# Kernel optimization log

Measured on AMD Instinct MI355X. Metric: run time of the kernel, lower is better.

Reference implementation:

```python
import jax, jax.numpy as jnp
import numpy as np
import math

B, T, D = 4, 8192, 1024
EPS = 1e-5

def setup_inputs() -> dict:
    key = jax.random.key(0)
    ks = jax.random.split(key, 8)
    xavier = lambda k, shape: jax.random.uniform(k, shape, jnp.float32,
                                                 -math.sqrt(6.0 / (shape[0] + shape[1])),
                                                 math.sqrt(6.0 / (shape[0] + shape[1])))
    x = jax.random.normal(ks[0], (B, T, D), jnp.float32)
    ln_gamma = jnp.ones((D,), jnp.float32)
    ln_beta = jnp.zeros((D,), jnp.float32)
    Wg = xavier(ks[1], (D, D))            # torch Linear weight: (out, in)
    bg = jnp.zeros((D,), jnp.float32)
    Wv = 0.01 * xavier(ks[2], (D, D))     # gain=0.01
    bv = jnp.zeros((D,), jnp.float32)
    Wo = 0.01 * xavier(ks[3], (D, D))     # gain=0.01
    bo = jnp.zeros((D,), jnp.float32)
    log_decay = jnp.asarray(math.log(math.exp(0.01) - 1.0), jnp.float32)
    return {"x": x, "ln_gamma": ln_gamma, "ln_beta": ln_beta,
            "Wg": Wg, "bg": bg, "Wv": Wv, "bv": bv, "Wo": Wo, "bo": bo,
            "log_decay": log_decay}

def reference(x, ln_gamma, ln_beta, Wg, bg, Wv, bv, Wo, bo, log_decay):
    # LayerNorm
    mu = jnp.mean(x, axis=-1, keepdims=True)
    var = jnp.mean(jnp.square(x - mu), axis=-1, keepdims=True)
    normed = (x - mu) * jax.lax.rsqrt(var + EPS) * ln_gamma + ln_beta
    # gate / value projections (torch Linear: y = x @ W.T + b)
    g = jax.nn.sigmoid(jnp.einsum('btd,ed->bte', normed, Wg) + bg)
    v = jnp.einsum('btd,ed->bte', normed, Wv) + bv
    # push-pull cumulative sums over time
    cumsum = jnp.cumsum(g * v, axis=1) - jnp.cumsum((1.0 - g) * v, axis=1)
    # positional exponential decay
    alpha = jax.nn.softplus(log_decay)
    positions = jnp.arange(x.shape[1], dtype=jnp.float32)
    decay = jnp.exp(-alpha * positions)[None, :, None]  # (1,T,1)
    out = jnp.einsum('btd,ed->bte', cumsum * decay, Wo) + bo
    return x + out  # dropout is identity at eval
```

## Files before the change

### kernel.cpp

```cpp
#include <hip/hip_runtime.h>
#include <cstdint>
#include <cstddef>

#define DD 1024
#define TT 8192
#define BB 4
#define MM (BB*TT)
#define NCHUNK 64
#define CLEN 128
#define EPS 1e-5f
#define NK2 16

typedef __attribute__((ext_vector_type(8))) short bf16x8;
typedef __attribute__((ext_vector_type(4))) float f32x4;

__device__ __forceinline__ float bf2f(unsigned short b) {
  union { unsigned int u; float f; } c; c.u = ((unsigned int)b) << 16; return c.f;
}
__device__ __forceinline__ unsigned short f2bf(float f) {
  union { float f; unsigned int u; } c; c.f = f;
  unsigned int lsb = (c.u >> 16) & 1u;
  c.u += 0x7fffu + lsb;
  return (unsigned short)(c.u >> 16);
}

__device__ __forceinline__ void gload16(const void* gsrc, void* ldst) {
  __builtin_amdgcn_global_load_lds(
      (const __attribute__((address_space(1))) unsigned int*)gsrc,
      (__attribute__((address_space(3))) unsigned int*)ldst, 16, 0, 0);
}

#define SWZ(row) (((row) >> 1) & 3)

__device__ __forceinline__ bf16x8 ldsfrag(const unsigned short* lds, int row, int sl) {
  int sp = sl ^ SWZ(row);
  return *(const bf16x8*)&lds[row * 32 + sp * 8];
}

#define MFMA16(a, b, c) __builtin_amdgcn_mfma_f32_16x16x32_bf16((a), (b), (c), 0, 0, 0)

#define VMCNT4 asm volatile("s_waitcnt vmcnt(4)" ::: "memory")
#define VMCNT0 asm volatile("s_waitcnt vmcnt(0)" ::: "memory")
#define BAR    __builtin_amdgcn_s_barrier()

__global__ __launch_bounds__(256) void cast_weights(
    const float* __restrict__ wg, const float* __restrict__ wv,
    const float* __restrict__ wo,
    unsigned short* __restrict__ owg, unsigned short* __restrict__ owv,
    unsigned short* __restrict__ owo) {
  int i = blockIdx.x * 256 + threadIdx.x;
  const float* src; unsigned short* dst; int off;
  if (i < 262144)       { src = wg; dst = owg; off = i; }
  else if (i < 524288)  { src = wv; dst = owv; off = i - 262144; }
  else                  { src = wo; dst = owo; off = i - 524288; }
  float4 v = ((const float4*)src)[off];
  ushort4 o;
  o.x = f2bf(v.x); o.y = f2bf(v.y); o.z = f2bf(v.z); o.w = f2bf(v.w);
  ((ushort4*)dst)[off] = o;
}

__global__ __launch_bounds__(256) void ln_kernel(
    const float* __restrict__ x, const float* __restrict__ gamma,
    const float* __restrict__ beta, unsigned short* __restrict__ normed) {
  size_t row = blockIdx.x;
  int tid = threadIdx.x, lane = tid & 63, wid = tid >> 6;
  float4 v = ((const float4*)(x + row * DD))[tid];
  float s = v.x + v.y + v.z + v.w;
  float q = v.x * v.x + v.y * v.y + v.z * v.z + v.w * v.w;
#pragma unroll
  for (int off = 32; off; off >>= 1) {
    s += __shfl_down(s, off);
    q += __shfl_down(q, off);
  }
  __shared__ float rs[4], rq[4];
  if (lane == 0) { rs[wid] = s; rq[wid] = q; }
  __syncthreads();
  float ts = rs[0] + rs[1] + rs[2] + rs[3];
  float tq = rq[0] + rq[1] + rq[2] + rq[3];
  float mu  = ts * (1.0f / DD);
  float var = tq * (1.0f / DD) - mu * mu;
  float rstd = rsqrtf(var + EPS);
  float4 gm = ((const float4*)gamma)[tid];
  float4 bt = ((const float4*)beta)[tid];
  ushort4 o;
  o.x = f2bf((v.x - mu) * rstd * gm.x + bt.x);
  o.y = f2bf((v.y - mu) * rstd * gm.y + bt.y);
  o.z = f2bf((v.z - mu) * rstd * gm.z + bt.z);
  o.w = f2bf((v.w - mu) * rstd * gm.w + bt.w);
  ((ushort4*)normed)[row * (DD / 4) + tid] = o;
}

__global__ __launch_bounds__(512, 2) void gemm_gv(
    const unsigned short* __restrict__ normed,
    const unsigned short* __restrict__ wg, const unsigned short* __restrict__ wv,
    const float* __restrict__ bg, const float* __restrict__ bv,
    unsigned short* __restrict__ u, float* __restrict__ sums) {
  __shared__ unsigned short As[2][2][256 * 32];
  __shared__ unsigned short Bgs[2][2][128 * 32];
  __shared__ unsigned short Bvs[2][2][128 * 32];
  int tid = threadIdx.x, lane = tid & 63, wid = tid >> 6;
  int wm = wid >> 2, wn = wid & 3;
  int nwg = gridDim.x;
  int swz = (blockIdx.x & 7) * (nwg >> 3) + (blockIdx.x >> 3);
  int bx = swz >> 3;
  int by = swz & 7;
  size_t m0 = (size_t)bx * 256;
  int n0 = by * 128;

  int rowq = tid >> 2, sp = tid & 3;
  int sl0 = sp ^ SWZ(rowq);
  const unsigned short* eA0 = normed + (m0 + rowq) * DD + sl0 * 8;
  const unsigned short* eA1 = normed + (m0 + 128 + rowq) * DD + sl0 * 8;
  const unsigned short* eBg = wg + ((size_t)n0 + rowq) * DD + sl0 * 8;
  const unsigned short* eBv = wv + ((size_t)n0 + rowq) * DD + sl0 * 8;

  auto SA = [&](int h) {
    char* d = (char*)&As[(h >> 1) & 1][h & 1][0] + tid * 16;
    gload16(eA0 + h * 32, d);
    gload16(eA1 + h * 32, d + 8192);
  };
  auto SB = [&](int h) {
    gload16(eBg + h * 32, (char*)&Bgs[(h >> 1) & 1][h & 1][0] + tid * 16);
    gload16(eBv + h * 32, (char*)&Bvs[(h >> 1) & 1][h & 1][0] + tid * 16);
  };

  f32x4 accg[8][2], accv[8][2];
#pragma unroll
  for (int a = 0; a < 8; ++a)
#pragma unroll
    for (int b = 0; b < 2; ++b) {
      accg[a][b] = (f32x4){0.f, 0.f, 0.f, 0.f};
      accv[a][b] = (f32x4){0.f, 0.f, 0.f, 0.f};
    }

  SA(0); SB(0); SA(1); SB(1);
  VMCNT4;
  BAR;

  int r = lane & 15, q = lane >> 4;
  for (int t = 0; t < NK2; ++t) {
    int buf = t & 1;
    bool more = (t + 1 < NK2);
    bf16x8 af[8], b0, b1;
    b0 = ldsfrag(Bgs[buf][0], wn * 32 + r, q);
    b1 = ldsfrag(Bgs[buf][0], wn * 32 + 16 + r, q);
#pragma unroll
    for (int mi = 0; mi < 8; ++mi)
      af[mi] = ldsfrag(As[buf][0], wm * 128 + mi * 16 + r, q);
    if (more) SA(2 * t + 2);
    BAR;
    __builtin_amdgcn_s_setprio(1);
#pragma unroll
    for (int mi = 0; mi < 8; ++mi) {
      accg[mi][0] = MFMA16(af[mi], b0, accg[mi][0]);
      accg[mi][1] = MFMA16(af[mi], b1, accg[mi][1]);
    }
    __builtin_amdgcn_s_setprio(0);
    BAR;
    b0 = ldsfrag(Bvs[buf][0], wn * 32 + r, q);
    b1 = ldsfrag(Bvs[buf][0], wn * 32 + 16 + r, q);
    if (more) SB(2 * t + 2);
    BAR;
    __builtin_amdgcn_s_setprio(1);
#pragma unroll
    for (int mi = 0; mi < 8; ++mi) {
      accv[mi][0] = MFMA16(af[mi], b0, accv[mi][0]);
      accv[mi][1] = MFMA16(af[mi], b1, accv[mi][1]);
    }
    __builtin_amdgcn_s_setprio(0);
    if (more) VMCNT4; else VMCNT0;
    BAR;
    b0 = ldsfrag(Bvs[buf][1], wn * 32 + r, q);
    b1 = ldsfrag(Bvs[buf][1], wn * 32 + 16 + r, q);
#pragma unroll
    for (int mi = 0; mi < 8; ++mi)
      af[mi] = ldsfrag(As[buf][1], wm * 128 + mi * 16 + r, q);
    if (more) SA(2 * t + 3);
    BAR;
    __builtin_amdgcn_s_setprio(1);
#pragma unroll
    for (int mi = 0; mi < 8; ++mi) {
      accv[mi][0] = MFMA16(af[mi], b0, accv[mi][0]);
      accv[mi][1] = MFMA16(af[mi], b1, accv[mi][1]);
    }
    __builtin_amdgcn_s_setprio(0);
    BAR;
    b0 = ldsfrag(Bgs[buf][1], wn * 32 + r, q);
    b1 = ldsfrag(Bgs[buf][1], wn * 32 + 16 + r, q);
    if (more) SB(2 * t + 3);
    BAR;
    __builtin_amdgcn_s_setprio(1);
#pragma unroll
    for (int mi = 0; mi < 8; ++mi) {
      accg[mi][0] = MFMA16(af[mi], b0, accg[mi][0]);
      accg[mi][1] = MFMA16(af[mi], b1, accg[mi][1]);
    }
    __builtin_amdgcn_s_setprio(0);
    if (more) VMCNT4;
    BAR;
  }

  float psum[2] = {0.f, 0.f};
#pragma unroll
  for (int mi = 0; mi < 8; ++mi)
#pragma unroll
    for (int ni = 0; ni < 2; ++ni) {
      int e = n0 + wn * 32 + ni * 16 + r;
      size_t rbase = m0 + wm * 128 + mi * 16 + q * 4;
      float bgv = bg[e], bvv = bv[e];
#pragma unroll
      for (int j = 0; j < 4; ++j) {
        float gp = accg[mi][ni][j] + bgv;
        float vp = accv[mi][ni][j] + bvv;
        float sg = 1.0f / (1.0f + __expf(-gp));
        float uu = (2.0f * sg - 1.0f) * vp;
        psum[ni] += uu;
        u[(rbase + j) * DD + e] = f2bf(uu);
      }
    }
#pragma unroll
  for (int ni = 0; ni < 2; ++ni) {
    psum[ni] += __shfl_xor(psum[ni], 16);
    psum[ni] += __shfl_xor(psum[ni], 32);
  }
  if (lane < 16) {
    int b = (int)(m0 >> 13);
    int ch = (int)((m0 & 8191) >> 7) + wm;
    size_t sidx = ((size_t)(b * NCHUNK + ch)) * DD + n0 + wn * 32 + lane;
    sums[sidx]      = psum[0];
    sums[sidx + 16] = psum[1];
  }
}

__global__ __launch_bounds__(256) void scan_chunks(float* __restrict__ sums) {
  int b = blockIdx.x >> 2;
  int e = (blockIdx.x & 3) * 256 + threadIdx.x;
  float vals[NCHUNK];
#pragma unroll
  for (int c = 0; c < NCHUNK; ++c)
    vals[c] = sums[((size_t)(b * NCHUNK + c)) * DD + e];
  float carry = 0.f;
#pragma unroll
  for (int c = 0; c < NCHUNK; ++c) {
    float t = vals[c]; vals[c] = carry; carry += t;
  }
#pragma unroll
  for (int c = 0; c < NCHUNK; ++c)
    sums[((size_t)(b * NCHUNK + c)) * DD + e] = vals[c];
}

__global__ __launch_bounds__(128) void scan_final(
    unsigned short* __restrict__ u, const float* __restrict__ sums,
    const float* __restrict__ log_decay) {
  int bid = blockIdx.x;
  int half = bid & 1, chunk = (bid >> 1) & 63, b = bid >> 7;
  int e0 = half * 512 + threadIdx.x * 4;
  float alpha = log1pf(__expf(log_decay[0]));
  float4 c = *(const float4*)(sums + ((size_t)(b * NCHUNK + chunk)) * DD + e0);
  size_t base = ((size_t)b * TT + (size_t)chunk * CLEN) * DD + e0;
#pragma unroll 4
  for (int i = 0; i < CLEN; ++i) {
    int t = chunk * CLEN + i;
    float dec = __expf(-alpha * (float)t);
    ushort4 w = *(const ushort4*)(u + base + (size_t)i * DD);
    c.x += bf2f(w.x); c.y += bf2f(w.y); c.z += bf2f(w.z); c.w += bf2f(w.w);
    ushort4 o;
    o.x = f2bf(c.x * dec); o.y = f2bf(c.y * dec);
    o.z = f2bf(c.z * dec); o.w = f2bf(c.w * dec);
    *(ushort4*)(u + base + (size_t)i * DD) = o;
  }
}

__global__ __launch_bounds__(512, 2) void gemm_out(
    const unsigned short* __restrict__ cmat, const unsigned short* __restrict__ wo,
    const float* __restrict__ bo, const float* __restrict__ x,
    float* __restrict__ out) {
  __shared__ unsigned short As[2][2][256 * 32];
  __shared__ unsigned short Bs[2][2][256 * 32];
  int tid = threadIdx.x, lane = tid & 63, wid = tid >> 6;
  int wm = wid >> 2, wn = wid & 3;
  int nwg = gridDim.x;
  int swz = (blockIdx.x & 7) * (nwg >> 3) + (blockIdx.x >> 3);
  int bx = swz >> 2;
  int by = swz & 3;
  size_t m0 = (size_t)bx * 256;
  int n0 = by * 256;

  int rowq = tid >> 2, sp = tid & 3;
  int sl0 = sp ^ SWZ(rowq);
  const unsigned short* eA0 = cmat + (m0 + rowq) * DD + sl0 * 8;
  const unsigned short* eA1 = cmat + (m0 + 128 + rowq) * DD + sl0 * 8;
  const unsigned short* eB0 = wo + ((size_t)n0 + rowq) * DD + sl0 * 8;
  const unsigned short* eB1 = wo + ((size_t)n0 + 128 + rowq) * DD + sl0 * 8;

  auto SA = [&](int h) {
    char* d = (char*)&As[(h >> 1) & 1][h & 1][0] + tid * 16;
    gload16(eA0 + h * 32, d);
    gload16(eA1 + h * 32, d + 8192);
  };
  auto SB = [&](int h) {
    char* d = (char*)&Bs[(h >> 1) & 1][h & 1][0] + tid * 16;
    gload16(eB0 + h * 32, d);
    gload16(eB1 + h * 32, d + 8192);
  };

  f32x4 acc[8][4];
#pragma unroll
  for (int a = 0; a < 8; ++a)
#pragma unroll
    for (int b = 0; b < 4; ++b) acc[a][b] = (f32x4){0.f, 0.f, 0.f, 0.f};

  SA(0); SB(0); SA(1); SB(1);
  VMCNT4;
  BAR;

  int r = lane & 15, q = lane >> 4;
  for (int t = 0; t < NK2; ++t) {
    int buf = t & 1;
    bool more = (t + 1 < NK2);
    bf16x8 af[8], b0, b1;
    b0 = ldsfrag(Bs[buf][0], wn * 64 + r, q);
    b1 = ldsfrag(Bs[buf][0], wn * 64 + 16 + r, q);
#pragma unroll
    for (int mi = 0; mi < 8; ++mi)
      af[mi] = ldsfrag(As[buf][0], wm * 128 + mi * 16 + r, q);
    if (more) SA(2 * t + 2);
    BAR;
    __builtin_amdgcn_s_setprio(1);
#pragma unroll
    for (int mi = 0; mi < 8; ++mi) {
      acc[mi][0] = MFMA16(af[mi], b0, acc[mi][0]);
      acc[mi][1] = MFMA16(af[mi], b1, acc[mi][1]);
    }
    __builtin_amdgcn_s_setprio(0);
    BAR;
    b0 = ldsfrag(Bs[buf][0], wn * 64 + 32 + r, q);
    b1 = ldsfrag(Bs[buf][0], wn * 64 + 48 + r, q);
    if (more) SB(2 * t + 2);
    BAR;
    __builtin_amdgcn_s_setprio(1);
#pragma unroll
    for (int mi = 0; mi < 8; ++mi) {
      acc[mi][2] = MFMA16(af[mi], b0, acc[mi][2]);
      acc[mi][3] = MFMA16(af[mi], b1, acc[mi][3]);
    }
    __builtin_amdgcn_s_setprio(0);
    if (more) VMCNT4; else VMCNT0;
    BAR;
    b0 = ldsfrag(Bs[buf][1], wn * 64 + r, q);
    b1 = ldsfrag(Bs[buf][1], wn * 64 + 16 + r, q);
#pragma unroll
    for (int mi = 0; mi < 8; ++mi)
      af[mi] = ldsfrag(As[buf][1], wm * 128 + mi * 16 + r, q);
    if (more) SA(2 * t + 3);
    BAR;
    __builtin_amdgcn_s_setprio(1);
#pragma unroll
    for (int mi = 0; mi < 8; ++mi) {
      acc[mi][0] = MFMA16(af[mi], b0, acc[mi][0]);
      acc[mi][1] = MFMA16(af[mi], b1, acc[mi][1]);
    }
    __builtin_amdgcn_s_setprio(0);
    BAR;
    b0 = ldsfrag(Bs[buf][1], wn * 64 + 32 + r, q);
    b1 = ldsfrag(Bs[buf][1], wn * 64 + 48 + r, q);
    if (more) SB(2 * t + 3);
    BAR;
    __builtin_amdgcn_s_setprio(1);
#pragma unroll
    for (int mi = 0; mi < 8; ++mi) {
      acc[mi][2] = MFMA16(af[mi], b0, acc[mi][2]);
      acc[mi][3] = MFMA16(af[mi], b1, acc[mi][3]);
    }
    __builtin_amdgcn_s_setprio(0);
    if (more) VMCNT4;
    BAR;
  }

#pragma unroll
  for (int mi = 0; mi < 8; ++mi)
#pragma unroll
    for (int nq = 0; nq < 4; ++nq) {
      int e = n0 + wn * 64 + nq * 16 + r;
      size_t rbase = m0 + wm * 128 + mi * 16 + q * 4;
      float bov = bo[e];
#pragma unroll
      for (int j = 0; j < 4; ++j) {
        size_t idx = (rbase + j) * DD + e;
        out[idx] = x[idx] + bov + acc[mi][nq][j];
      }
    }
}

extern "C" void kernel_launch(void* const* d_in, const int* in_sizes, int n_in,
                              void* d_out, int out_size, void* d_ws, size_t ws_size,
                              hipStream_t stream) {
  const float* x     = (const float*)d_in[0];
  const float* gamma = (const float*)d_in[1];
  const float* beta  = (const float*)d_in[2];
  const float* Wg    = (const float*)d_in[3];
  const float* bg    = (const float*)d_in[4];
  const float* Wv    = (const float*)d_in[5];
  const float* bv    = (const float*)d_in[6];
  const float* Wo    = (const float*)d_in[7];
  const float* bo    = (const float*)d_in[8];
  const float* ldcy  = (const float*)d_in[9];
  float* out = (float*)d_out;

  char* ws = (char*)d_ws;
  unsigned short* normed = (unsigned short*)ws;
  unsigned short* u      = (unsigned short*)(ws + (size_t)67108864);
  unsigned short* wgb    = (unsigned short*)(ws + (size_t)134217728);
  unsigned short* wvb    = wgb + 1048576;
  unsigned short* wob    = wvb + 1048576;
  float* sums            = (float*)(ws + (size_t)134217728 + (size_t)3 * 2097152);

  cast_weights<<<3072, 256, 0, stream>>>(Wg, Wv, Wo, wgb, wvb, wob);
  ln_kernel<<<MM, 256, 0, stream>>>(x, gamma, beta, normed);
  gemm_gv<<<dim3(MM / 256 * (DD / 128)), 512, 0, stream>>>(normed, wgb, wvb, bg, bv, u, sums);
  scan_chunks<<<BB * (DD / 256), 256, 0, stream>>>(sums);
  scan_final<<<BB * NCHUNK * 2, 128, 0, stream>>>(u, sums, ldcy);
  gemm_out<<<dim3(MM / 256 * (DD / 256)), 512, 0, stream>>>(u, wob, bo, x, out);
}
```

Measured before the change: 321.3 us.

## Load A fragments directly from global into registers, staging only weights in LDS

Both GEMMs stop staging the activation (A) tile through LDS. Each wave now reads its A fragments straight from global memory into registers, double-buffered across half-k steps, and only the weight tiles still go through LDS via global_load_lds. The loop is restructured to fewer barriers per k-iteration with a full vmcnt(0) wait, aiming to cut LDS traffic, LDS footprint and barrier overhead. The risks are uncoalesced 16-byte-per-lane global reads for A with no reuse across the four wn waves, which fetch the same rows redundantly, and a coarser wait that can expose global latency.

```diff
diff --git a/kernel.cpp b/kernel.cpp
--- a/kernel.cpp
+++ b/kernel.cpp
@@ -39,7 +39,6 @@
 
 #define MFMA16(a, b, c) __builtin_amdgcn_mfma_f32_16x16x32_bf16((a), (b), (c), 0, 0, 0)
 
-#define VMCNT4 asm volatile("s_waitcnt vmcnt(4)" ::: "memory")
 #define VMCNT0 asm volatile("s_waitcnt vmcnt(0)" ::: "memory")
 #define BAR    __builtin_amdgcn_s_barrier()
 
@@ -95,7 +94,6 @@
     const unsigned short* __restrict__ wg, const unsigned short* __restrict__ wv,
     const float* __restrict__ bg, const float* __restrict__ bv,
     unsigned short* __restrict__ u, float* __restrict__ sums) {
-  __shared__ unsigned short As[2][2][256 * 32];
   __shared__ unsigned short Bgs[2][2][128 * 32];
   __shared__ unsigned short Bvs[2][2][128 * 32];
   int tid = threadIdx.x, lane = tid & 63, wid = tid >> 6;
@@ -109,20 +107,18 @@
 
   int rowq = tid >> 2, sp = tid & 3;
   int sl0 = sp ^ SWZ(rowq);
-  const unsigned short* eA0 = normed + (m0 + rowq) * DD + sl0 * 8;
-  const unsigned short* eA1 = normed + (m0 + 128 + rowq) * DD + sl0 * 8;
   const unsigned short* eBg = wg + ((size_t)n0 + rowq) * DD + sl0 * 8;
   const unsigned short* eBv = wv + ((size_t)n0 + rowq) * DD + sl0 * 8;
-
-  auto SA = [&](int h) {
-    char* d = (char*)&As[(h >> 1) & 1][h & 1][0] + tid * 16;
-    gload16(eA0 + h * 32, d);
-    gload16(eA1 + h * 32, d + 8192);
+  auto SB = [&](int t1) {
+    int k0 = t1 * 64;
+    gload16(eBg + k0,      (char*)&Bgs[t1 & 1][0][0] + tid * 16);
+    gload16(eBv + k0,      (char*)&Bvs[t1 & 1][0][0] + tid * 16);
+    gload16(eBg + k0 + 32, (char*)&Bgs[t1 & 1][1][0] + tid * 16);
+    gload16(eBv + k0 + 32, (char*)&Bvs[t1 & 1][1][0] + tid * 16);
   };
-  auto SB = [&](int h) {
-    gload16(eBg + h * 32, (char*)&Bgs[(h >> 1) & 1][h & 1][0] + tid * 16);
-    gload16(eBv + h * 32, (char*)&Bvs[(h >> 1) & 1][h & 1][0] + tid * 16);
-  };
+
+  int r = lane & 15, q = lane >> 4;
+  const unsigned short* aBase = normed + (m0 + wm * 128 + r) * DD + q * 8;
 
   f32x4 accg[8][2], accv[8][2];
 #pragma unroll
@@ -133,71 +129,54 @@
       accv[a][b] = (f32x4){0.f, 0.f, 0.f, 0.f};
     }
 
-  SA(0); SB(0); SA(1); SB(1);
-  VMCNT4;
+  bf16x8 af0[8], af1[8];
+  SB(0);
+#pragma unroll
+  for (int mi = 0; mi < 8; ++mi)
+    af0[mi] = *(const bf16x8*)(aBase + (size_t)mi * 16 * DD);
+  VMCNT0;
   BAR;
 
-  int r = lane & 15, q = lane >> 4;
   for (int t = 0; t < NK2; ++t) {
     int buf = t & 1;
     bool more = (t + 1 < NK2);
-    bf16x8 af[8], b0, b1;
-    b0 = ldsfrag(Bgs[buf][0], wn * 32 + r, q);
-    b1 = ldsfrag(Bgs[buf][0], wn * 32 + 16 + r, q);
+    bf16x8 g0, g1, v0, v1;
+    if (more) SB(t + 1);
+    g0 = ldsfrag(Bgs[buf][0], wn * 32 + r, q);
+    g1 = ldsfrag(Bgs[buf][0], wn * 32 + 16 + r, q);
+    v0 = ldsfrag(Bvs[buf][0], wn * 32 + r, q);
+    v1 = ldsfrag(Bvs[buf][0], wn * 32 + 16 + r, q);
 #pragma unroll
     for (int mi = 0; mi < 8; ++mi)
-      af[mi] = ldsfrag(As[buf][0], wm * 128 + mi * 16 + r, q);
-    if (more) SA(2 * t + 2);
-    BAR;
+      af1[mi] = *(const bf16x8*)(aBase + (size_t)mi * 16 * DD + t * 64 + 32);
     __builtin_amdgcn_s_setprio(1);
 #pragma unroll
     for (int mi = 0; mi < 8; ++mi) {
-      accg[mi][0] = MFMA16(af[mi], b0, accg[mi][0]);
-      accg[mi][1] = MFMA16(af[mi], b1, accg[mi][1]);
+      accg[mi][0] = MFMA16(af0[mi], g0, accg[mi][0]);
+      accg[mi][1] = MFMA16(af0[mi], g1, accg[mi][1]);
+      accv[mi][0] = MFMA16(af0[mi], v0, accv[mi][0]);
+      accv[mi][1] = MFMA16(af0[mi], v1, accv[mi][1]);
     }
     __builtin_amdgcn_s_setprio(0);
-    BAR;
-    b0 = ldsfrag(Bvs[buf][0], wn * 32 + r, q);
-    b1 = ldsfrag(Bvs[buf][0], wn * 32 + 16 + r, q);
-    if (more) SB(2 * t + 2);
-    BAR;
+    g0 = ldsfrag(Bgs[buf][1], wn * 32 + r, q);
+    g1 = ldsfrag(Bgs[buf][1], wn * 32 + 16 + r, q);
+    v0 = ldsfrag(Bvs[buf][1], wn * 32 + r, q);
+    v1 = ldsfrag(Bvs[buf][1], wn * 32 + 16 + r, q);
+    if (more) {
+#pragma unroll
+      for (int mi = 0; mi < 8; ++mi)
+        af0[mi] = *(const bf16x8*)(aBase + (size_t)mi * 16 * DD + (t + 1) * 64);
+    }
     __builtin_amdgcn_s_setprio(1);
 #pragma unroll
     for (int mi = 0; mi < 8; ++mi) {
-      accv[mi][0] = MFMA16(af[mi], b0, accv[mi][0]);
-      accv[mi][1] = MFMA16(af[mi], b1, accv[mi][1]);
+      accg[mi][0] = MFMA16(af1[mi], g0, accg[mi][0]);
+      accg[mi][1] = MFMA16(af1[mi], g1, accg[mi][1]);
+      accv[mi][0] = MFMA16(af1[mi], v0, accv[mi][0]);
+      accv[mi][1] = MFMA16(af1[mi], v1, accv[mi][1]);
     }
     __builtin_amdgcn_s_setprio(0);
-    if (more) VMCNT4; else VMCNT0;
-    BAR;
-    b0 = ldsfrag(Bvs[buf][1], wn * 32 + r, q);
-    b1 = ldsfrag(Bvs[buf][1], wn * 32 + 16 + r, q);
-#pragma unroll
-    for (int mi = 0; mi < 8; ++mi)
-      af[mi] = ldsfrag(As[buf][1], wm * 128 + mi * 16 + r, q);
-    if (more) SA(2 * t + 3);
-    BAR;
-    __builtin_amdgcn_s_setprio(1);
-#pragma unroll
-    for (int mi = 0; mi < 8; ++mi) {
-      accv[mi][0] = MFMA16(af[mi], b0, accv[mi][0]);
-      accv[mi][1] = MFMA16(af[mi], b1, accv[mi][1]);
-    }
-    __builtin_amdgcn_s_setprio(0);
-    BAR;
-    b0 = ldsfrag(Bgs[buf][1], wn * 32 + r, q);
-    b1 = ldsfrag(Bgs[buf][1], wn * 32 + 16 + r, q);
-    if (more) SB(2 * t + 3);
-    BAR;
-    __builtin_amdgcn_s_setprio(1);
-#pragma unroll
-    for (int mi = 0; mi < 8; ++mi) {
-      accg[mi][0] = MFMA16(af[mi], b0, accg[mi][0]);
-      accg[mi][1] = MFMA16(af[mi], b1, accg[mi][1]);
-    }
-    __builtin_amdgcn_s_setprio(0);
-    if (more) VMCNT4;
-    BAR;
+    if (more) { VMCNT0; BAR; }
   }
 
   float psum[2] = {0.f, 0.f};
@@ -275,7 +254,6 @@
     const unsigned short* __restrict__ cmat, const unsigned short* __restrict__ wo,
     const float* __restrict__ bo, const float* __restrict__ x,
     float* __restrict__ out) {
-  __shared__ unsigned short As[2][2][256 * 32];
   __shared__ unsigned short Bs[2][2][256 * 32];
   int tid = threadIdx.x, lane = tid & 63, wid = tid >> 6;
   int wm = wid >> 2, wn = wid & 3;
@@ -288,21 +266,20 @@
 
   int rowq = tid >> 2, sp = tid & 3;
   int sl0 = sp ^ SWZ(rowq);
-  const unsigned short* eA0 = cmat + (m0 + rowq) * DD + sl0 * 8;
-  const unsigned short* eA1 = cmat + (m0 + 128 + rowq) * DD + sl0 * 8;
   const unsigned short* eB0 = wo + ((size_t)n0 + rowq) * DD + sl0 * 8;
   const unsigned short* eB1 = wo + ((size_t)n0 + 128 + rowq) * DD + sl0 * 8;
-
-  auto SA = [&](int h) {
-    char* d = (char*)&As[(h >> 1) & 1][h & 1][0] + tid * 16;
-    gload16(eA0 + h * 32, d);
-    gload16(eA1 + h * 32, d + 8192);
+  auto SB = [&](int t1) {
+    int k0 = t1 * 64;
+    char* d0 = (char*)&Bs[t1 & 1][0][0] + tid * 16;
+    char* d1 = (char*)&Bs[t1 & 1][1][0] + tid * 16;
+    gload16(eB0 + k0,      d0);
+    gload16(eB1 + k0,      d0 + 8192);
+    gload16(eB0 + k0 + 32, d1);
+    gload16(eB1 + k0 + 32, d1 + 8192);
   };
-  auto SB = [&](int h) {
-    char* d = (char*)&Bs[(h >> 1) & 1][h & 1][0] + tid * 16;
-    gload16(eB0 + h * 32, d);
-    gload16(eB1 + h * 32, d + 8192);
-  };
+
+  int r = lane & 15, q = lane >> 4;
+  const unsigned short* aBase = cmat + (m0 + wm * 128 + r) * DD + q * 8;
 
   f32x4 acc[8][4];
 #pragma unroll
@@ -310,71 +287,54 @@
 #pragma unroll
     for (int b = 0; b < 4; ++b) acc[a][b] = (f32x4){0.f, 0.f, 0.f, 0.f};
 
-  SA(0); SB(0); SA(1); SB(1);
-  VMCNT4;
+  bf16x8 af0[8], af1[8];
+  SB(0);
+#pragma unroll
+  for (int mi = 0; mi < 8; ++mi)
+    af0[mi] = *(const bf16x8*)(aBase + (size_t)mi * 16 * DD);
+  VMCNT0;
   BAR;
 
-  int r = lane & 15, q = lane >> 4;
   for (int t = 0; t < NK2; ++t) {
     int buf = t & 1;
     bool more = (t + 1 < NK2);
-    bf16x8 af[8], b0, b1;
+    bf16x8 b0, b1, b2, b3;
+    if (more) SB(t + 1);
     b0 = ldsfrag(Bs[buf][0], wn * 64 + r, q);
     b1 = ldsfrag(Bs[buf][0], wn * 64 + 16 + r, q);
+    b2 = ldsfrag(Bs[buf][0], wn * 64 + 32 + r, q);
+    b3 = ldsfrag(Bs[buf][0], wn * 64 + 48 + r, q);
 #pragma unroll
     for (int mi = 0; mi < 8; ++mi)
-      af[mi] = ldsfrag(As[buf][0], wm * 128 + mi * 16 + r, q);
-    if (more) SA(2 * t + 2);
-    BAR;
+      af1[mi] = *(const bf16x8*)(aBase + (size_t)mi * 16 * DD + t * 64 + 32);
     __builtin_amdgcn_s_setprio(1);
 #pragma unroll
     for (int mi = 0; mi < 8; ++mi) {
-      acc[mi][0] = MFMA16(af[mi], b0, acc[mi][0]);
-      acc[mi][1] = MFMA16(af[mi], b1, acc[mi][1]);
+      acc[mi][0] = MFMA16(af0[mi], b0, acc[mi][0]);
+      acc[mi][1] = MFMA16(af0[mi], b1, acc[mi][1]);
+      acc[mi][2] = MFMA16(af0[mi], b2, acc[mi][2]);
+      acc[mi][3] = MFMA16(af0[mi], b3, acc[mi][3]);
     }
     __builtin_amdgcn_s_setprio(0);
-    BAR;
-    b0 = ldsfrag(Bs[buf][0], wn * 64 + 32 + r, q);
-    b1 = ldsfrag(Bs[buf][0], wn * 64 + 48 + r, q);
-    if (more) SB(2 * t + 2);
-    BAR;
-    __builtin_amdgcn_s_setprio(1);
-#pragma unroll
-    for (int mi = 0; mi < 8; ++mi) {
-      acc[mi][2] = MFMA16(af[mi], b0, acc[mi][2]);
-      acc[mi][3] = MFMA16(af[mi], b1, acc[mi][3]);
-    }
-    __builtin_amdgcn_s_setprio(0);
-    if (more) VMCNT4; else VMCNT0;
-    BAR;
     b0 = ldsfrag(Bs[buf][1], wn * 64 + r, q);
     b1 = ldsfrag(Bs[buf][1], wn * 64 + 16 + r, q);
-#pragma unroll
-    for (int mi = 0; mi < 8; ++mi)
-      af[mi] = ldsfrag(As[buf][1], wm * 128 + mi * 16 + r, q);
-    if (more) SA(2 * t + 3);
-    BAR;
+    b2 = ldsfrag(Bs[buf][1], wn * 64 + 32 + r, q);
+    b3 = ldsfrag(Bs[buf][1], wn * 64 + 48 + r, q);
+    if (more) {
+#pragma unroll
+      for (int mi = 0; mi < 8; ++mi)
+        af0[mi] = *(const bf16x8*)(aBase + (size_t)mi * 16 * DD + (t + 1) * 64);
+    }
     __builtin_amdgcn_s_setprio(1);
 #pragma unroll
     for (int mi = 0; mi < 8; ++mi) {
-      acc[mi][0] = MFMA16(af[mi], b0, acc[mi][0]);
-      acc[mi][1] = MFMA16(af[mi], b1, acc[mi][1]);
+      acc[mi][0] = MFMA16(af1[mi], b0, acc[mi][0]);
+      acc[mi][1] = MFMA16(af1[mi], b1, acc[mi][1]);
+      acc[mi][2] = MFMA16(af1[mi], b2, acc[mi][2]);
+      acc[mi][3] = MFMA16(af1[mi], b3, acc[mi][3]);
     }
     __builtin_amdgcn_s_setprio(0);
-    BAR;
-    b0 = ldsfrag(Bs[buf][1], wn * 64 + 32 + r, q);
-    b1 = ldsfrag(Bs[buf][1], wn * 64 + 48 + r, q);
-    if (more) SB(2 * t + 3);
-    BAR;
-    __builtin_amdgcn_s_setprio(1);
-#pragma unroll
-    for (int mi = 0; mi < 8; ++mi) {
-      acc[mi][2] = MFMA16(af[mi], b0, acc[mi][2]);
-      acc[mi][3] = MFMA16(af[mi], b1, acc[mi][3]);
-    }
-    __builtin_amdgcn_s_setprio(0);
-    if (more) VMCNT4;
-    BAR;
+    if (more) { VMCNT0; BAR; }
   }
 
 #pragma unroll
```

New measurement: 548.9 us. +70.8%, slower.

## Switch both GEMMs to 32x32x16 MFMA with precomputed LDS fragment pointers

Applied to the files above, without the earlier changes.

Both projection GEMMs now use the 32x32x16 bf16 MFMA instead of 16x16x32. Each wave issues half as many MFMA instructions and fewer LDS fragment reads, and fragment addresses are precomputed once so the loop uses immediate offsets. The epilogues are rewritten for the 32x32 accumulator layout. Separately, the scan kernel replaces a per-step exp with a running multiplicative decay, which trades one transcendental per step for slight accumulated rounding drift.

```diff
diff --git a/kernel.cpp b/kernel.cpp
--- a/kernel.cpp
+++ b/kernel.cpp
@@ -13,6 +13,7 @@
 
 typedef __attribute__((ext_vector_type(8))) short bf16x8;
 typedef __attribute__((ext_vector_type(4))) float f32x4;
+typedef __attribute__((ext_vector_type(16))) float f32x16;
 
 __device__ __forceinline__ float bf2f(unsigned short b) {
   union { unsigned int u; float f; } c; c.u = ((unsigned int)b) << 16; return c.f;
@@ -32,16 +33,16 @@
 
 #define SWZ(row) (((row) >> 1) & 3)
 
-__device__ __forceinline__ bf16x8 ldsfrag(const unsigned short* lds, int row, int sl) {
-  int sp = sl ^ SWZ(row);
-  return *(const bf16x8*)&lds[row * 32 + sp * 8];
-}
-
-#define MFMA16(a, b, c) __builtin_amdgcn_mfma_f32_16x16x32_bf16((a), (b), (c), 0, 0, 0)
-
+#define MFMA32(a, b, c) __builtin_amdgcn_mfma_f32_32x32x16_bf16((a), (b), (c), 0, 0, 0)
+#define BAR    __builtin_amdgcn_s_barrier()
+#define PRIO1  __builtin_amdgcn_s_setprio(1)
+#define PRIO0  __builtin_amdgcn_s_setprio(0)
 #define VMCNT4 asm volatile("s_waitcnt vmcnt(4)" ::: "memory")
 #define VMCNT0 asm volatile("s_waitcnt vmcnt(0)" ::: "memory")
-#define BAR    __builtin_amdgcn_s_barrier()
+
+__device__ __forceinline__ bf16x8 LDI(const char* p, int imm) {
+  return *(const bf16x8*)(p + imm);
+}
 
 __global__ __launch_bounds__(256) void cast_weights(
     const float* __restrict__ wg, const float* __restrict__ wv,
@@ -94,7 +95,7 @@
     const unsigned short* __restrict__ normed,
     const unsigned short* __restrict__ wg, const unsigned short* __restrict__ wv,
     const float* __restrict__ bg, const float* __restrict__ bv,
-    unsigned short* __restrict__ u, float* __restrict__ sums) {
+    unsigned short* __restrict__ uout, float* __restrict__ sums) {
   __shared__ unsigned short As[2][2][256 * 32];
   __shared__ unsigned short Bgs[2][2][128 * 32];
   __shared__ unsigned short Bvs[2][2][128 * 32];
@@ -113,7 +114,6 @@
   const unsigned short* eA1 = normed + (m0 + 128 + rowq) * DD + sl0 * 8;
   const unsigned short* eBg = wg + ((size_t)n0 + rowq) * DD + sl0 * 8;
   const unsigned short* eBv = wv + ((size_t)n0 + rowq) * DD + sl0 * 8;
-
   auto SA = [&](int h) {
     char* d = (char*)&As[(h >> 1) & 1][h & 1][0] + tid * 16;
     gload16(eA0 + h * 32, d);
@@ -124,111 +124,121 @@
     gload16(eBv + h * 32, (char*)&Bvs[(h >> 1) & 1][h & 1][0] + tid * 16);
   };
 
-  f32x4 accg[8][2], accv[8][2];
-#pragma unroll
-  for (int a = 0; a < 8; ++a)
-#pragma unroll
-    for (int b = 0; b < 2; ++b) {
-      accg[a][b] = (f32x4){0.f, 0.f, 0.f, 0.f};
-      accv[a][b] = (f32x4){0.f, 0.f, 0.f, 0.f};
-    }
+  f32x16 accg[4], accv[4];
+#pragma unroll
+  for (int a = 0; a < 4; ++a)
+#pragma unroll
+    for (int k = 0; k < 16; ++k) { accg[a][k] = 0.f; accv[a][k] = 0.f; }
 
   SA(0); SB(0); SA(1); SB(1);
   VMCNT4;
   BAR;
 
-  int r = lane & 15, q = lane >> 4;
+  int r32 = lane & 31, q2 = lane >> 5;
+  int swl = (r32 >> 1) & 3;
+  int phys0 = (q2 ^ swl) << 4;
+  const char* pA[2][2][2];
+  const char* pG[2][2][2];
+  const char* pV[2][2][2];
+#pragma unroll
+  for (int d = 0; d < 2; ++d)
+#pragma unroll
+    for (int kh = 0; kh < 2; ++kh) {
+      const char* a0 = (const char*)&As[d][kh][0] + (wm * 128 + r32) * 64 + phys0;
+      const char* g0 = (const char*)&Bgs[d][kh][0] + (wn * 32 + r32) * 64 + phys0;
+      const char* v0 = (const char*)&Bvs[d][kh][0] + (wn * 32 + r32) * 64 + phys0;
+      pA[d][kh][0] = a0; pA[d][kh][1] = (const char*)((uintptr_t)a0 ^ 32);
+      pG[d][kh][0] = g0; pG[d][kh][1] = (const char*)((uintptr_t)g0 ^ 32);
+      pV[d][kh][0] = v0; pV[d][kh][1] = (const char*)((uintptr_t)v0 ^ 32);
+    }
+
+  bf16x8 af[4][2], bf0, bf1;
   for (int t = 0; t < NK2; ++t) {
     int buf = t & 1;
     bool more = (t + 1 < NK2);
-    bf16x8 af[8], b0, b1;
-    b0 = ldsfrag(Bgs[buf][0], wn * 32 + r, q);
-    b1 = ldsfrag(Bgs[buf][0], wn * 32 + 16 + r, q);
-#pragma unroll
-    for (int mi = 0; mi < 8; ++mi)
-      af[mi] = ldsfrag(As[buf][0], wm * 128 + mi * 16 + r, q);
+#pragma unroll
+    for (int mi = 0; mi < 4; ++mi)
+#pragma unroll
+      for (int ks = 0; ks < 2; ++ks)
+        af[mi][ks] = LDI(pA[buf][0][ks], mi * 2048);
+    bf0 = LDI(pG[buf][0][0], 0);
+    bf1 = LDI(pG[buf][0][1], 0);
     if (more) SA(2 * t + 2);
     BAR;
-    __builtin_amdgcn_s_setprio(1);
-#pragma unroll
-    for (int mi = 0; mi < 8; ++mi) {
-      accg[mi][0] = MFMA16(af[mi], b0, accg[mi][0]);
-      accg[mi][1] = MFMA16(af[mi], b1, accg[mi][1]);
-    }
-    __builtin_amdgcn_s_setprio(0);
-    BAR;
-    b0 = ldsfrag(Bvs[buf][0], wn * 32 + r, q);
-    b1 = ldsfrag(Bvs[buf][0], wn * 32 + 16 + r, q);
+    PRIO1;
+#pragma unroll
+    for (int mi = 0; mi < 4; ++mi) {
+      accg[mi] = MFMA32(af[mi][0], bf0, accg[mi]);
+      accg[mi] = MFMA32(af[mi][1], bf1, accg[mi]);
+    }
+    PRIO0;
+    BAR;
+    bf0 = LDI(pV[buf][0][0], 0);
+    bf1 = LDI(pV[buf][0][1], 0);
     if (more) SB(2 * t + 2);
     BAR;
-    __builtin_amdgcn_s_setprio(1);
-#pragma unroll
-    for (int mi = 0; mi < 8; ++mi) {
-      accv[mi][0] = MFMA16(af[mi], b0, accv[mi][0]);
-      accv[mi][1] = MFMA16(af[mi], b1, accv[mi][1]);
-    }
-    __builtin_amdgcn_s_setprio(0);
+    PRIO1;
+#pragma unroll
+    for (int mi = 0; mi < 4; ++mi) {
+      accv[mi] = MFMA32(af[mi][0], bf0, accv[mi]);
+      accv[mi] = MFMA32(af[mi][1], bf1, accv[mi]);
+    }
+    PRIO0;
     if (more) VMCNT4; else VMCNT0;
     BAR;
-    b0 = ldsfrag(Bvs[buf][1], wn * 32 + r, q);
-    b1 = ldsfrag(Bvs[buf][1], wn * 32 + 16 + r, q);
-#pragma unroll
-    for (int mi = 0; mi < 8; ++mi)
-      af[mi] = ldsfrag(As[buf][1], wm * 128 + mi * 16 + r, q);
+#pragma unroll
+    for (int mi = 0; mi < 4; ++mi)
+#pragma unroll
+      for (int ks = 0; ks < 2; ++ks)
+        af[mi][ks] = LDI(pA[buf][1][ks], mi * 2048);
+    bf0 = LDI(pV[buf][1][0], 0);
+    bf1 = LDI(pV[buf][1][1], 0);
     if (more) SA(2 * t + 3);
     BAR;
-    __builtin_amdgcn_s_setprio(1);
-#pragma unroll
-    for (int mi = 0; mi < 8; ++mi) {
-      accv[mi][0] = MFMA16(af[mi], b0, accv[mi][0]);
-      accv[mi][1] = MFMA16(af[mi], b1, accv[mi][1]);
-    }
-    __builtin_amdgcn_s_setprio(0);
-    BAR;
-    b0 = ldsfrag(Bgs[buf][1], wn * 32 + r, q);
-    b1 = ldsfrag(Bgs[buf][1], wn * 32 + 16 + r, q);
+    PRIO1;
+#pragma unroll
+    for (int mi = 0; mi < 4; ++mi) {
+      accv[mi] = MFMA32(af[mi][0], bf0, accv[mi]);
+      accv[mi] = MFMA32(af[mi][1], bf1, accv[mi]);
+    }
+    PRIO0;
+    BAR;
+    bf0 = LDI(pG[buf][1][0], 0);
+    bf1 = LDI(pG[buf][1][1], 0);
     if (more) SB(2 * t + 3);
     BAR;
-    __builtin_amdgcn_s_setprio(1);
-#pragma unroll
-    for (int mi = 0; mi < 8; ++mi) {
-      accg[mi][0] = MFMA16(af[mi], b0, accg[mi][0]);
-      accg[mi][1] = MFMA16(af[mi], b1, accg[mi][1]);
-    }
-    __builtin_amdgcn_s_setprio(0);
+    PRIO1;
+#pragma unroll
+    for (int mi = 0; mi < 4; ++mi) {
+      accg[mi] = MFMA32(af[mi][0], bf0, accg[mi]);
+      accg[mi] = MFMA32(af[mi][1], bf1, accg[mi]);
+    }
+    PRIO0;
     if (more) VMCNT4;
     BAR;
   }
 
-  float psum[2] = {0.f, 0.f};
-#pragma unroll
-  for (int mi = 0; mi < 8; ++mi)
-#pragma unroll
-    for (int ni = 0; ni < 2; ++ni) {
-      int e = n0 + wn * 32 + ni * 16 + r;
-      size_t rbase = m0 + wm * 128 + mi * 16 + q * 4;
-      float bgv = bg[e], bvv = bv[e];
-#pragma unroll
-      for (int j = 0; j < 4; ++j) {
-        float gp = accg[mi][ni][j] + bgv;
-        float vp = accv[mi][ni][j] + bvv;
-        float sg = 1.0f / (1.0f + __expf(-gp));
-        float uu = (2.0f * sg - 1.0f) * vp;
-        psum[ni] += uu;
-        u[(rbase + j) * DD + e] = f2bf(uu);
-      }
-    }
-#pragma unroll
-  for (int ni = 0; ni < 2; ++ni) {
-    psum[ni] += __shfl_xor(psum[ni], 16);
-    psum[ni] += __shfl_xor(psum[ni], 32);
-  }
-  if (lane < 16) {
+  int e = n0 + wn * 32 + r32;
+  float bgv = bg[e], bvv = bv[e];
+  float psum = 0.f;
+#pragma unroll
+  for (int mi = 0; mi < 4; ++mi)
+#pragma unroll
+    for (int reg = 0; reg < 16; ++reg) {
+      int rowin = (reg & 3) + 8 * (reg >> 2) + 4 * q2;
+      size_t row = m0 + wm * 128 + mi * 32 + rowin;
+      float gp = accg[mi][reg] + bgv;
+      float vp = accv[mi][reg] + bvv;
+      float sg = 1.0f / (1.0f + __expf(-gp));
+      float uu = (2.0f * sg - 1.0f) * vp;
+      psum += uu;
+      uout[row * DD + e] = f2bf(uu);
+    }
+  psum += __shfl_xor(psum, 32);
+  if (lane < 32) {
     int b = (int)(m0 >> 13);
     int ch = (int)((m0 & 8191) >> 7) + wm;
-    size_t sidx = ((size_t)(b * NCHUNK + ch)) * DD + n0 + wn * 32 + lane;
-    sums[sidx]      = psum[0];
-    sums[sidx + 16] = psum[1];
+    sums[((size_t)(b * NCHUNK + ch)) * DD + e] = psum;
   }
 }
 
@@ -256,18 +266,19 @@
   int half = bid & 1, chunk = (bid >> 1) & 63, b = bid >> 7;
   int e0 = half * 512 + threadIdx.x * 4;
   float alpha = log1pf(__expf(log_decay[0]));
+  float dec  = __expf(-alpha * (float)(chunk * CLEN));
+  float step = __expf(-alpha);
   float4 c = *(const float4*)(sums + ((size_t)(b * NCHUNK + chunk)) * DD + e0);
   size_t base = ((size_t)b * TT + (size_t)chunk * CLEN) * DD + e0;
 #pragma unroll 4
   for (int i = 0; i < CLEN; ++i) {
-    int t = chunk * CLEN + i;
-    float dec = __expf(-alpha * (float)t);
     ushort4 w = *(const ushort4*)(u + base + (size_t)i * DD);
     c.x += bf2f(w.x); c.y += bf2f(w.y); c.z += bf2f(w.z); c.w += bf2f(w.w);
     ushort4 o;
     o.x = f2bf(c.x * dec); o.y = f2bf(c.y * dec);
     o.z = f2bf(c.z * dec); o.w = f2bf(c.w * dec);
     *(ushort4*)(u + base + (size_t)i * DD) = o;
+    dec *= step;
   }
 }
 
@@ -292,7 +303,6 @@
   const unsigned short* eA1 = cmat + (m0 + 128 + rowq) * DD + sl0 * 8;
   const unsigned short* eB0 = wo + ((size_t)n0 + rowq) * DD + sl0 * 8;
   const unsigned short* eB1 = wo + ((size_t)n0 + 128 + rowq) * DD + sl0 * 8;
-
   auto SA = [&](int h) {
     char* d = (char*)&As[(h >> 1) & 1][h & 1][0] + tid * 16;
     gload16(eA0 + h * 32, d);
@@ -304,92 +314,112 @@
     gload16(eB1 + h * 32, d + 8192);
   };
 
-  f32x4 acc[8][4];
-#pragma unroll
-  for (int a = 0; a < 8; ++a)
-#pragma unroll
-    for (int b = 0; b < 4; ++b) acc[a][b] = (f32x4){0.f, 0.f, 0.f, 0.f};
+  f32x16 acc[4][2];
+#pragma unroll
+  for (int a = 0; a < 4; ++a)
+#pragma unroll
+    for (int n = 0; n < 2; ++n)
+#pragma unroll
+      for (int k = 0; k < 16; ++k) acc[a][n][k] = 0.f;
 
   SA(0); SB(0); SA(1); SB(1);
   VMCNT4;
   BAR;
 
-  int r = lane & 15, q = lane >> 4;
+  int r32 = lane & 31, q2 = lane >> 5;
+  int swl = (r32 >> 1) & 3;
+  int phys0 = (q2 ^ swl) << 4;
+  const char* pA[2][2][2];
+  const char* pB[2][2][2];
+#pragma unroll
+  for (int d = 0; d < 2; ++d)
+#pragma unroll
+    for (int kh = 0; kh < 2; ++kh) {
+      const char* a0 = (const char*)&As[d][kh][0] + (wm * 128 + r32) * 64 + phys0;
+      const char* b0 = (const char*)&Bs[d][kh][0] + (wn * 64 + r32) * 64 + phys0;
+      pA[d][kh][0] = a0; pA[d][kh][1] = (const char*)((uintptr_t)a0 ^ 32);
+      pB[d][kh][0] = b0; pB[d][kh][1] = (const char*)((uintptr_t)b0 ^ 32);
+    }
+
+  bf16x8 af[4][2], b0f, b1f;
   for (int t = 0; t < NK2; ++t) {
     int buf = t & 1;
     bool more = (t + 1 < NK2);
-    bf16x8 af[8], b0, b1;
-    b0 = ldsfrag(Bs[buf][0], wn * 64 + r, q);
-    b1 = ldsfrag(Bs[buf][0], wn * 64 + 16 + r, q);
-#pragma unroll
-    for (int mi = 0; mi < 8; ++mi)
-      af[mi] = ldsfrag(As[buf][0], wm * 128 + mi * 16 + r, q);
+#pragma unroll
+    for (int mi = 0; mi < 4; ++mi)
+#pragma unroll
+      for (int ks = 0; ks < 2; ++ks)
+        af[mi][ks] = LDI(pA[buf][0][ks], mi * 2048);
+    b0f = LDI(pB[buf][0][0], 0);
+    b1f = LDI(pB[buf][0][1], 0);
     if (more) SA(2 * t + 2);
     BAR;
-    __builtin_amdgcn_s_setprio(1);
-#pragma unroll
-    for (int mi = 0; mi < 8; ++mi) {
-      acc[mi][0] = MFMA16(af[mi], b0, acc[mi][0]);
-      acc[mi][1] = MFMA16(af[mi], b1, acc[mi][1]);
-    }
-    __builtin_amdgcn_s_setprio(0);
-    BAR;
-    b0 = ldsfrag(Bs[buf][0], wn * 64 + 32 + r, q);
-    b1 = ldsfrag(Bs[buf][0], wn * 64 + 48 + r, q);
+    PRIO1;
+#pragma unroll
+    for (int mi = 0; mi < 4; ++mi) {
+      acc[mi][0] = MFMA32(af[mi][0], b0f, acc[mi][0]);
+      acc[mi][0] = MFMA32(af[mi][1], b1f, acc[mi][0]);
+    }
+    PRIO0;
+    BAR;
+    b0f = LDI(pB[buf][0][0], 2048);
+    b1f = LDI(pB[buf][0][1], 2048);
     if (more) SB(2 * t + 2);
     BAR;
-    __builtin_amdgcn_s_setprio(1);
-#pragma unroll
-    for (int mi = 0; mi < 8; ++mi) {
-      acc[mi][2] = MFMA16(af[mi], b0, acc[mi][2]);
-      acc[mi][3] = MFMA16(af[mi], b1, acc[mi][3]);
-    }
-    __builtin_amdgcn_s_setprio(0);
+    PRIO1;
+#pragma unroll
+    for (int mi = 0; mi < 4; ++mi) {
+      acc[mi][1] = MFMA32(af[mi][0], b0f, acc[mi][1]);
+      acc[mi][1] = MFMA32(af[mi][1], b1f, acc[mi][1]);
+    }
+    PRIO0;
     if (more) VMCNT4; else VMCNT0;
     BAR;
-    b0 = ldsfrag(Bs[buf][1], wn * 64 + r, q);
-    b1 = ldsfrag(Bs[buf][1], wn * 64 + 16 + r, q);
-#pragma unroll
-    for (int mi = 0; mi < 8; ++mi)
-      af[mi] = ldsfrag(As[buf][1], wm * 128 + mi * 16 + r, q);
+#pragma unroll
+    for (int mi = 0; mi < 4; ++mi)
+#pragma unroll
+      for (int ks = 0; ks < 2; ++ks)
+        af[mi][ks] = LDI(pA[buf][1][ks], mi * 2048);
+    b0f = LDI(pB[buf][1][0], 0);
+    b1f = LDI(pB[buf][1][1], 0);
     if (more) SA(2 * t + 3);
     BAR;
-    __builtin_amdgcn_s_setprio(1);
-#pragma unroll
-    for (int mi = 0; mi < 8; ++mi) {
-      acc[mi][0] = MFMA16(af[mi], b0, acc[mi][0]);
-      acc[mi][1] = MFMA16(af[mi], b1, acc[mi][1]);
-    }
-    __builtin_amdgcn_s_setprio(0);
-    BAR;
-    b0 = ldsfrag(Bs[buf][1], wn * 64 + 32 + r, q);
-    b1 = ldsfrag(Bs[buf][1], wn * 64 + 48 + r, q);
+    PRIO1;
+#pragma unroll
+    for (int mi = 0; mi < 4; ++mi) {
+      acc[mi][0] = MFMA32(af[mi][0], b0f, acc[mi][0]);
+      acc[mi][0] = MFMA32(af[mi][1], b1f, acc[mi][0]);
+    }
+    PRIO0;
+    BAR;
+    b0f = LDI(pB[buf][1][0], 2048);
+    b1f = LDI(pB[buf][1][1], 2048);
     if (more) SB(2 * t + 3);
     BAR;
-    __builtin_amdgcn_s_setprio(1);
-#pragma unroll
-    for (int mi = 0; mi < 8; ++mi) {
-      acc[mi][2] = MFMA16(af[mi], b0, acc[mi][2]);
-      acc[mi][3] = MFMA16(af[mi], b1, acc[mi][3]);
-    }
-    __builtin_amdgcn_s_setprio(0);
+    PRIO1;
+#pragma unroll
+    for (int mi = 0; mi < 4; ++mi) {
+      acc[mi][1] = MFMA32(af[mi][0], b0f, acc[mi][1]);
+      acc[mi][1] = MFMA32(af[mi][1], b1f, acc[mi][1]);
+    }
+    PRIO0;
     if (more) VMCNT4;
     BAR;
   }
 
 #pragma unroll
-  for (int mi = 0; mi < 8; ++mi)
-#pragma unroll
-    for (int nq = 0; nq < 4; ++nq) {
-      int e = n0 + wn * 64 + nq * 16 + r;
-      size_t rbase = m0 + wm * 128 + mi * 16 + q * 4;
-      float bov = bo[e];
-#pragma unroll
-      for (int j = 0; j < 4; ++j) {
-        size_t idx = (rbase + j) * DD + e;
-        out[idx] = x[idx] + bov + acc[mi][nq][j];
+  for (int nj = 0; nj < 2; ++nj) {
+    int e = n0 + wn * 64 + nj * 32 + r32;
+    float bov = bo[e];
+#pragma unroll
+    for (int mi = 0; mi < 4; ++mi)
+#pragma unroll
+      for (int reg = 0; reg < 16; ++reg) {
+        int rowin = (reg & 3) + 8 * (reg >> 2) + 4 * q2;
+        size_t idx = (m0 + wm * 128 + mi * 32 + rowin) * DD + e;
+        out[idx] = x[idx] + bov + acc[mi][nj][reg];
       }
-    }
+  }
 }
 
 extern "C" void kernel_launch(void* const* d_in, const int* in_sizes, int n_in,
```

Result: slower. 512.1 us (+59.4%).
